# Kernel tuning notes

Measured on AMD Instinct MI355X. Metric: run time of the kernel, lower is better.

Reference implementation:

```python
import jax, jax.numpy as jnp
import numpy as np

S = 4        # support_num
NEI = 32     # neighbor_num for conv stages
POOL_NEI = 4 # neighbor_num inside Pool_layer
EPS = 1e-12


def sq_dist(a, b):
    # a: (b,m,3), b: (b,n,3) -> (b,m,n)
    return (jnp.sum(a * a, -1)[:, :, None] + jnp.sum(b * b, -1)[:, None, :]
            - 2.0 * jnp.einsum('bmd,bnd->bmn', a, b))


def query_ball(radius, k, points, queries):
    # PointNet++-style ball query: up to k indices within radius, padded with first hit.
    d = sq_dist(queries, points)                      # (b,m,n)
    n = points.shape[1]
    idx = jnp.broadcast_to(jnp.arange(n, dtype=jnp.int32), d.shape)
    idx = jnp.where(d > radius * radius, n, idx)
    idx = jnp.sort(idx, axis=-1)[..., :k]             # (b,m,k)
    first = idx[..., :1]
    return jnp.where(idx == n, first, idx)


def gather_nb(feat, idx):
    # feat: (b,v,c), idx: (b,v,k) -> (b,v,k,c)
    return jax.vmap(lambda f, i: f[i])(feat, idx)


def neighbor_dir_norm(verts, idx):
    nb = gather_nb(verts, idx)                        # (b,v,k,3)
    d = nb - verts[:, :, None, :]
    return d / (jnp.linalg.norm(d, axis=-1, keepdims=True) + EPS)


def conv_surface(idx, verts, dirs):
    # dirs: (3, S*out). Geometric-only first layer of 3DGCN.
    b, v, k = idx.shape
    o = dirs.shape[1] // S
    dn = neighbor_dir_norm(verts, idx)                # (b,v,k,3)
    sd = dirs / (jnp.linalg.norm(dirs, axis=0, keepdims=True) + EPS)
    theta = jnp.maximum(jnp.einsum('bvkd,dm->bvkm', dn, sd), 0.0)
    theta = theta.reshape(b, v, k, S, o)
    return theta.max(axis=2).sum(axis=2)              # (b,v,o)


def conv_layer(idx, verts, feat, w, bias, dirs):
    # w: (cin,(S+1)*o), bias: ((S+1)*o,), dirs: (3,S*o)
    b, v, k = idx.shape
    o = dirs.shape[1] // S
    dn = neighbor_dir_norm(verts, idx)
    sd = dirs / (jnp.linalg.norm(dirs, axis=0, keepdims=True) + EPS)
    theta = jnp.maximum(jnp.einsum('bvkd,dm->bvkm', dn, sd), 0.0)  # (b,v,k,S*o)
    fout = feat @ w + bias                            # (b,v,(S+1)*o)
    center, supp = fout[..., :o], fout[..., o:]
    supp_nb = gather_nb(supp, idx)                    # (b,v,k,S*o)
    act = (theta * supp_nb).reshape(b, v, k, S, o).max(axis=2).sum(axis=2)
    return center + act


def pool(verts, feat, radius):
    idx = query_ball(radius, POOL_NEI, verts, verts)
    pooled = gather_nb(feat, idx).max(axis=2)         # (b,v,c)
    m = verts.shape[1] // 2                           # pooling_rate = 2 (deterministic subsample)
    return verts[:, :m], pooled[:, :m]


def setup_inputs() -> dict:
    key = jax.random.key(0)
    ks = jax.random.split(key, 32)
    B, V = 4, 4096
    inp = {}
    inp['vertices'] = jax.random.uniform(ks[0], (B, V, 3), dtype=jnp.float32)
    inp['surf_dirs'] = jax.random.normal(ks[1], (3, S * 32), dtype=jnp.float32) * 0.1
    specs = [(1, 32, 32), (3, 64, 32), (4, 96, 32), (6, 128, 32), (7, 160, 32),
             (8, 192, 32), (9, 224, 32), (10, 256, 32), (11, 288, 1024)]
    i = 2
    for n, cin, cout in specs:
        inp[f'w{n}'] = jax.random.normal(ks[i], (cin, (S + 1) * cout), dtype=jnp.float32) / np.sqrt(cin); i += 1
        inp[f'b{n}'] = jnp.zeros(((S + 1) * cout,), jnp.float32)
        inp[f'd{n}'] = jax.random.normal(ks[i], (3, S * cout), dtype=jnp.float32) * 0.1; i += 1
    inp['fc1_w'] = jax.random.normal(ks[i], (1024, 256), dtype=jnp.float32) * 0.03; i += 1
    inp['fc1_b'] = jnp.zeros((256,), jnp.float32)
    inp['bn_g'] = jnp.ones((256,), jnp.float32)
    inp['bn_b'] = jnp.zeros((256,), jnp.float32)
    inp['bn_m'] = jnp.zeros((256,), jnp.float32)
    inp['bn_v'] = jnp.ones((256,), jnp.float32)
    inp['fc2_w'] = jax.random.normal(ks[i], (256, 40), dtype=jnp.float32) * 0.06
    inp['fc2_b'] = jnp.zeros((40,), jnp.float32)
    return inp


def reference(vertices, surf_dirs, w1, b1, d1, w3, b3, d3, w4, b4, d4, w6, b6, d6,
              w7, b7, d7, w8, b8, d8, w9, b9, d9, w10, b10, d10, w11, b11, d11,
              fc1_w, fc1_b, bn_g, bn_b, bn_m, bn_v, fc2_w, fc2_b):
    relu = lambda x: jnp.maximum(x, 0.0)
    verts = vertices
    idx = query_ball(0.2, NEI, verts, verts)
    fm0 = relu(conv_surface(idx, verts, surf_dirs))
    fm1 = relu(conv_layer(idx, verts, fm0, w1, b1, d1))
    fm1 = jnp.concatenate([fm0, fm1], -1)
    verts, fm1 = pool(verts, fm1, 0.2)
    idx = query_ball(0.4, NEI, verts, verts)
    fm3 = relu(conv_layer(idx, verts, fm1, w3, b3, d3)); fm3 = jnp.concatenate([fm1, fm3], -1)
    fm4 = relu(conv_layer(idx, verts, fm3, w4, b4, d4)); fm4 = jnp.concatenate([fm3, fm4], -1)
    verts, fm4 = pool(verts, fm4, 0.4)
    idx = query_ball(0.6, NEI, verts, verts)
    fm6 = relu(conv_layer(idx, verts, fm4, w6, b6, d6)); fm6 = jnp.concatenate([fm4, fm6], -1)
    fm7 = relu(conv_layer(idx, verts, fm6, w7, b7, d7)); fm7 = jnp.concatenate([fm6, fm7], -1)
    verts, fm7 = pool(verts, fm7, 0.6)
    idx = query_ball(0.8, NEI, verts, verts)
    fm8 = relu(conv_layer(idx, verts, fm7, w8, b8, d8)); fm8 = jnp.concatenate([fm7, fm8], -1)
    fm9 = relu(conv_layer(idx, verts, fm8, w9, b9, d9)); fm9 = jnp.concatenate([fm8, fm9], -1)
    verts, fm9 = pool(verts, fm9, 0.8)
    idx = query_ball(1.0, NEI, verts, verts)
    fm10 = relu(conv_layer(idx, verts, fm9, w10, b10, d10)); fm10 = jnp.concatenate([fm9, fm10], -1)
    fm11 = conv_layer(idx, verts, fm10, w11, b11, d11)
    g = fm11.max(axis=1)                              # (b,1024) global max pool
    h = g @ fc1_w + fc1_b                             # Dropout is identity at inference
    h = (h - bn_m) / jnp.sqrt(bn_v + 1e-5) * bn_g + bn_b
    h = relu(h)
    return h @ fc2_w + fc2_b                          # (b,40)
```

## Files before the change

### kernel.cpp

```cpp
#include <hip/hip_runtime.h>
#include <hip/hip_bf16.h>
#include <math.h>

#define DEV __device__ __forceinline__

DEV float frn_mul(float a, float b) { return __fmul_rn(a, b); }
DEV float frn_add(float a, float b) { return __fadd_rn(a, b); }

union BFU { __hip_bfloat16 h; unsigned short u; };

typedef __attribute__((ext_vector_type(8))) short short8v;
typedef __attribute__((ext_vector_type(4))) float f32x4;

__global__ void pack4_kernel(const float* __restrict__ v, float4* __restrict__ out,
                             int n)
{
    int t = blockIdx.x * blockDim.x + threadIdx.x;
    if (t >= n) return;
    float x = v[(size_t)t * 3 + 0], y = v[(size_t)t * 3 + 1], z = v[(size_t)t * 3 + 2];
    float pn = frn_add(frn_add(frn_mul(x, x), frn_mul(y, y)), frn_mul(z, z));
    out[t] = make_float4(x, y, z, pn);
}

__global__ void qb_kernel(const float4* __restrict__ pts4all, int Vp, int Vq, int B,
                          float r2, int K, int* __restrict__ idx_out)
{
    int wid = (blockIdx.x * blockDim.x + threadIdx.x) >> 6;
    int lane = threadIdx.x & 63;
    int nq = B * Vq;
    if (wid >= nq) return;
    int b = wid / Vq;
    int v = wid - b * Vq;

    float4 q4 = pts4all[(size_t)b * Vp + v];
    float qx = q4.x, qy = q4.y, qz = q4.z, qn = q4.w;
    const float4* pts = pts4all + (size_t)b * Vp;
    int* row = idx_out + (size_t)wid * K;

    int count = 0;
    int first = -1;
    float4 p = pts[lane];
    for (int base = 0; base < Vp && count < K; base += 64) {
        int jn = base + 64 + lane;
        float4 pnext = pts[jn < Vp ? jn : 0];
        float dt = frn_add(frn_add(frn_mul(qx, p.x), frn_mul(qy, p.y)), frn_mul(qz, p.z));
        float d = __fsub_rn(frn_add(qn, p.w), frn_mul(2.0f, dt));
        bool in = !(d > r2);
        unsigned long long mask = __ballot(in);
        if (first < 0 && mask != 0ull)
            first = base + (int)__ffsll((long long)mask) - 1;
        int pos = count + (int)__popcll(mask & ((1ull << lane) - 1ull));
        if (in && pos < K) row[pos] = base + lane;
        count += (int)__popcll(mask);
        p = pnext;
    }
    int cnt = count < K ? count : K;
    for (int t = cnt + lane; t < K; t += 64) row[t] = first;
}

__global__ void qb_surface_kernel(const float4* __restrict__ pts4all, int V, int B,
                                  float r2,
                                  const float* __restrict__ dirs,
                                  float* __restrict__ outF, int Cw,
                                  int* __restrict__ idx_out)
{
    __shared__ int rowS[4][32];
    int wid = (blockIdx.x * blockDim.x + threadIdx.x) >> 6;
    int lane = threadIdx.x & 63;
    int wql = threadIdx.x >> 6;
    int b = wid / V;

    float4 q4 = pts4all[(size_t)wid];
    float qx = q4.x, qy = q4.y, qz = q4.z, qn = q4.w;
    const float4* pts = pts4all + (size_t)b * V;
    int* row = idx_out + (size_t)wid * 32;

    int count = 0;
    int first = -1;
    float4 p = pts[lane];
    for (int base = 0; base < V && count < 32; base += 64) {
        int jn = base + 64 + lane;
        float4 pnext = pts[jn < V ? jn : 0];
        float dt = frn_add(frn_add(frn_mul(qx, p.x), frn_mul(qy, p.y)), frn_mul(qz, p.z));
        float d = __fsub_rn(frn_add(qn, p.w), frn_mul(2.0f, dt));
        bool in = !(d > r2);
        unsigned long long mask = __ballot(in);
        if (first < 0 && mask != 0ull)
            first = base + (int)__ffsll((long long)mask) - 1;
        int pos = count + (int)__popcll(mask & ((1ull << lane) - 1ull));
        if (in && pos < 32) { row[pos] = base + lane; rowS[wql][pos] = base + lane; }
        count += (int)__popcll(mask);
        p = pnext;
    }
    int cnt = count < 32 ? count : 32;
    for (int t = cnt + lane; t < 32; t += 64) { row[t] = first; rowS[wql][t] = first; }
    __syncthreads();

    float dnx, dny, dnz;
    {
        int k = lane & 31;
        float4 nb4 = pts[rowS[wql][k]];
        float dx = nb4.x - qx;
        float dy = nb4.y - qy;
        float dz = nb4.z - qz;
        float nrm = sqrtf(dx * dx + dy * dy + dz * dz) + 1e-12f;
        float inv = 1.0f / nrm;
        dnx = dx * inv; dny = dy * inv; dnz = dz * inv;
    }
    int m1 = lane, m2 = lane + 64;
    float ax = dirs[m1], ay = dirs[128 + m1], az = dirs[256 + m1];
    float i1 = 1.0f / (sqrtf(ax * ax + ay * ay + az * az) + 1e-12f);
    ax *= i1; ay *= i1; az *= i1;
    float bx = dirs[m2], by = dirs[128 + m2], bz = dirs[256 + m2];
    float i2 = 1.0f / (sqrtf(bx * bx + by * by + bz * bz) + 1e-12f);
    bx *= i2; by *= i2; bz *= i2;

    float mx1 = -INFINITY, mx2 = -INFINITY;
    for (int k = 0; k < 32; ++k) {
        float ex = __shfl(dnx, k, 64);
        float ey = __shfl(dny, k, 64);
        float ez = __shfl(dnz, k, 64);
        float t1 = fmaxf(ex * ax + ey * ay + ez * az, 0.0f);
        float t2 = fmaxf(ex * bx + ey * by + ez * bz, 0.0f);
        mx1 = fmaxf(mx1, t1);
        mx2 = fmaxf(mx2, t2);
    }
    float part = mx1 + mx2;
    float tot = part + __shfl_xor(part, 32, 64);
    if (lane < 32) {
        outF[(size_t)wid * Cw + lane] = fmaxf(tot, 0.0f);
    }
}

template <typename OT>
__global__ __launch_bounds__(256)
void gemm_tiled_kernel(const float* __restrict__ feat, int Cw, int cin,
                       const float* __restrict__ w, const float* __restrict__ bias,
                       int N, OT* __restrict__ fout)
{
    __shared__ float As[64][36];
    __shared__ float Bs[32][68];

    int m0 = blockIdx.x * 64;
    int n0 = blockIdx.y * 64;
    int tid = threadIdx.x;
    int tx = tid & 15, ty = tid >> 4;

    float acc[4][4];
#pragma unroll
    for (int i = 0; i < 4; ++i)
#pragma unroll
        for (int j = 0; j < 4; ++j) acc[i][j] = 0.0f;

    for (int k0 = 0; k0 < cin; k0 += 32) {
#pragma unroll
        for (int i = 0; i < 2; ++i) {
            int qq = tid + i * 256;
            int row = qq >> 3, c = qq & 7;
            float4 v = *(const float4*)&feat[(size_t)(m0 + row) * Cw + k0 + 4 * c];
            *(float4*)&As[row][4 * c] = v;
        }
#pragma unroll
        for (int i = 0; i < 2; ++i) {
            int qq = tid + i * 256;
            int kr = qq >> 4, c = qq & 15;
            int n = n0 + 4 * c;
            float4 v = make_float4(0.0f, 0.0f, 0.0f, 0.0f);
            if (n < N) v = *(const float4*)&w[(size_t)(k0 + kr) * N + n];
            *(float4*)&Bs[kr][4 * c] = v;
        }
        __syncthreads();

#pragma unroll
        for (int kt = 0; kt < 32; kt += 4) {
            float4 av4[4], bv4[4];
#pragma unroll
            for (int i = 0; i < 4; ++i) av4[i] = *(const float4*)&As[ty * 4 + i][kt];
#pragma unroll
            for (int r = 0; r < 4; ++r) bv4[r] = *(const float4*)&Bs[kt + r][tx * 4];
            const float* a = (const float*)av4;
            const float* bb = (const float*)bv4;
#pragma unroll
            for (int i = 0; i < 4; ++i)
#pragma unroll
                for (int r = 0; r < 4; ++r)
#pragma unroll
                    for (int j = 0; j < 4; ++j)
                        acc[i][j] = fmaf(a[i * 4 + r], bb[r * 4 + j], acc[i][j]);
        }
        __syncthreads();
    }

    int n = n0 + tx * 4;
    if (n < N) {
        float b0 = bias[n + 0], b1 = bias[n + 1], b2 = bias[n + 2], b3 = bias[n + 3];
#pragma unroll
        for (int i = 0; i < 4; ++i) {
            int m = m0 + ty * 4 + i;
            if constexpr (__is_same(OT, float)) {
                float4 o;
                o.x = acc[i][0] + b0;
                o.y = acc[i][1] + b1;
                o.z = acc[i][2] + b2;
                o.w = acc[i][3] + b3;
                *(float4*)&fout[(size_t)m * N + n] = o;
            } else {
                BFU t0, t1, t2, t3;
                t0.h = __float2bfloat16(acc[i][0] + b0);
                t1.h = __float2bfloat16(acc[i][1] + b1);
                t2.h = __float2bfloat16(acc[i][2] + b2);
                t3.h = __float2bfloat16(acc[i][3] + b3);
                ushort4 o;
                o.x = t0.u; o.y = t1.u; o.z = t2.u; o.w = t3.u;
                *(ushort4*)&fout[(size_t)m * N + n] = o;
            }
        }
    }
}

__global__ void cast_bf16_kernel(const float* __restrict__ src,
                                 unsigned short* __restrict__ dst, int n8)
{
    int t = blockIdx.x * blockDim.x + threadIdx.x;
    if (t >= n8) return;
    float4 v0 = *(const float4*)&src[(size_t)t * 8];
    float4 v1 = *(const float4*)&src[(size_t)t * 8 + 4];
    BFU a;
    ushort4 o0, o1;
    a.h = __float2bfloat16(v0.x); o0.x = a.u;
    a.h = __float2bfloat16(v0.y); o0.y = a.u;
    a.h = __float2bfloat16(v0.z); o0.z = a.u;
    a.h = __float2bfloat16(v0.w); o0.w = a.u;
    a.h = __float2bfloat16(v1.x); o1.x = a.u;
    a.h = __float2bfloat16(v1.y); o1.y = a.u;
    a.h = __float2bfloat16(v1.z); o1.z = a.u;
    a.h = __float2bfloat16(v1.w); o1.w = a.u;
    *(ushort4*)&dst[(size_t)t * 8] = o0;
    *(ushort4*)&dst[(size_t)t * 8 + 4] = o1;
}

__global__ void castT_bf16_kernel(const float* __restrict__ w,
                                  unsigned short* __restrict__ wt)
{
    int t = blockIdx.x * blockDim.x + threadIdx.x;
    if (t >= 5120 * 36) return;
    int kc = t / 5120;
    int n = t - kc * 5120;
    BFU a;
    ushort4 o0, o1;
    a.h = __float2bfloat16(w[(size_t)(kc * 8 + 0) * 5120 + n]); o0.x = a.u;
    a.h = __float2bfloat16(w[(size_t)(kc * 8 + 1) * 5120 + n]); o0.y = a.u;
    a.h = __float2bfloat16(w[(size_t)(kc * 8 + 2) * 5120 + n]); o0.z = a.u;
    a.h = __float2bfloat16(w[(size_t)(kc * 8 + 3) * 5120 + n]); o0.w = a.u;
    a.h = __float2bfloat16(w[(size_t)(kc * 8 + 4) * 5120 + n]); o1.x = a.u;
    a.h = __float2bfloat16(w[(size_t)(kc * 8 + 5) * 5120 + n]); o1.y = a.u;
    a.h = __float2bfloat16(w[(size_t)(kc * 8 + 6) * 5120 + n]); o1.z = a.u;
    a.h = __float2bfloat16(w[(size_t)(kc * 8 + 7) * 5120 + n]); o1.w = a.u;
    *(ushort4*)&wt[(size_t)n * 288 + kc * 8] = o0;
    *(ushort4*)&wt[(size_t)n * 288 + kc * 8 + 4] = o1;
}

__global__ __launch_bounds__(256)
void gemm_mfma_conv11(const unsigned short* __restrict__ Abf,
                      const unsigned short* __restrict__ WTbf,
                      const float* __restrict__ bias,
                      __hip_bfloat16* __restrict__ fout)
{
    __shared__ unsigned short As[128][40];
    __shared__ unsigned short Bs[128][40];
    const int K = 288, N = 5120;
    int m0 = blockIdx.x * 128;
    int n0 = blockIdx.y * 128;
    int tid = threadIdx.x;
    int lane = tid & 63;
    int wave = tid >> 6;
    int wm = wave & 1, wn = wave >> 1;
    int l15 = lane & 15, l4 = lane >> 4;

    f32x4 acc[4][4];
#pragma unroll
    for (int mi = 0; mi < 4; ++mi)
#pragma unroll
        for (int ni = 0; ni < 4; ++ni) acc[mi][ni] = (f32x4){0.f, 0.f, 0.f, 0.f};

    for (int k0 = 0; k0 < K; k0 += 32) {
#pragma unroll
        for (int i = 0; i < 2; ++i) {
            int c = tid + i * 256;
            int row = c >> 2, qq = c & 3;
            *(uint4*)&As[row][qq * 8] = *(const uint4*)&Abf[(size_t)(m0 + row) * K + k0 + qq * 8];
            *(uint4*)&Bs[row][qq * 8] = *(const uint4*)&WTbf[(size_t)(n0 + row) * K + k0 + qq * 8];
        }
        __syncthreads();

        short8v af[4], bfv[4];
#pragma unroll
        for (int mi = 0; mi < 4; ++mi)
            af[mi] = *(const short8v*)&As[wm * 64 + mi * 16 + l15][l4 * 8];
#pragma unroll
        for (int ni = 0; ni < 4; ++ni)
            bfv[ni] = *(const short8v*)&Bs[wn * 64 + ni * 16 + l15][l4 * 8];
#pragma unroll
        for (int mi = 0; mi < 4; ++mi)
#pragma unroll
            for (int ni = 0; ni < 4; ++ni)
                acc[mi][ni] = __builtin_amdgcn_mfma_f32_16x16x32_bf16(af[mi], bfv[ni], acc[mi][ni], 0, 0, 0);
        __syncthreads();
    }

#pragma unroll
    for (int ni = 0; ni < 4; ++ni) {
        int col = n0 + wn * 64 + ni * 16 + l15;
        float bv = bias[col];
#pragma unroll
        for (int mi = 0; mi < 4; ++mi) {
            int rbase = m0 + wm * 64 + mi * 16 + l4 * 4;
#pragma unroll
            for (int j = 0; j < 4; ++j) {
                BFU u;
                u.h = __float2bfloat16(acc[mi][ni][j] + bv);
                *(unsigned short*)&fout[(size_t)(rbase + j) * N + col] = u.u;
            }
        }
    }
}

__global__ void conv_agg32_kernel(const int* __restrict__ idx,
                                  const float4* __restrict__ verts4,
                                  const float* __restrict__ fout,
                                  const float* __restrict__ dirs,
                                  float* __restrict__ outF, int Cw, int coff,
                                  int V, int do_relu)
{
    int blk = blockIdx.x;
    int b = (blk & 7) >> 1;
    int j = ((blk >> 3) << 1) | (blk & 1);
    int wid = b * V + j * 4 + (int)(threadIdx.x >> 6);
    int lane = threadIdx.x & 63;

    float dnx, dny, dnz;
    int nbrow;
    {
        int k = lane & 31;
        int nb = idx[(size_t)wid * 32 + k];
        nbrow = b * V + nb;
        float4 c4 = verts4[(size_t)wid];
        float4 n4 = verts4[(size_t)nbrow];
        float dx = n4.x - c4.x;
        float dy = n4.y - c4.y;
        float dz = n4.z - c4.z;
        float nrm = sqrtf(dx * dx + dy * dy + dz * dz) + 1e-12f;
        float inv = 1.0f / nrm;
        dnx = dx * inv; dny = dy * inv; dnz = dz * inv;
    }
    int m1 = lane, m2 = lane + 64;
    float ax = dirs[m1], ay = dirs[128 + m1], az = dirs[256 + m1];
    float i1 = 1.0f / (sqrtf(ax * ax + ay * ay + az * az) + 1e-12f);
    ax *= i1; ay *= i1; az *= i1;
    float bx = dirs[m2], by = dirs[128 + m2], bz = dirs[256 + m2];
    float i2 = 1.0f / (sqrtf(bx * bx + by * by + bz * bz) + 1e-12f);
    bx *= i2; by *= i2; bz *= i2;

    float a1[4] = {-INFINITY, -INFINITY, -INFINITY, -INFINITY};
    float a2[4] = {-INFINITY, -INFINITY, -INFINITY, -INFINITY};
#pragma unroll
    for (int kk = 0; kk < 32; kk += 4) {
#pragma unroll
        for (int u = 0; u < 4; ++u) {
            int k = kk + u;
            float ex = __shfl(dnx, k, 64);
            float ey = __shfl(dny, k, 64);
            float ez = __shfl(dnz, k, 64);
            int nr = __shfl(nbrow, k, 64);
            const float* fr = fout + (size_t)nr * 160 + 32;
            float t1 = fmaxf(ex * ax + ey * ay + ez * az, 0.0f);
            float t2 = fmaxf(ex * bx + ey * by + ez * bz, 0.0f);
            a1[u] = fmaxf(a1[u], t1 * fr[m1]);
            a2[u] = fmaxf(a2[u], t2 * fr[m2]);
        }
    }
    float mx1 = fmaxf(fmaxf(a1[0], a1[1]), fmaxf(a1[2], a1[3]));
    float mx2 = fmaxf(fmaxf(a2[0], a2[1]), fmaxf(a2[2], a2[3]));
    float part = mx1 + mx2;
    float tot = part + __shfl_xor(part, 32, 64);
    if (lane < 32) {
        float c = fout[(size_t)wid * 160 + lane];
        float val = c + tot;
        if (do_relu) val = fmaxf(val, 0.0f);
        outF[(size_t)wid * Cw + coff + lane] = val;
    }
}

__global__ void conv_agg_big_kernel(const int* __restrict__ idx,
                                    const float4* __restrict__ verts4,
                                    const __hip_bfloat16* __restrict__ fout,
                                    const float* __restrict__ dirs,
                                    float* __restrict__ G,
                                    int V, int B)
{
    __shared__ float dnS[32][3];
    __shared__ int nbS[32];
    int blk = blockIdx.x;
    int b = (blk & 7) >> 1;
    int v = ((blk >> 3) << 1) | (blk & 1);
    int row = b * V + v;
    int tid = threadIdx.x;

    if (tid < 32) {
        int nb = idx[(size_t)row * 32 + tid];
        int nbrow = b * V + nb;
        float4 c4 = verts4[(size_t)row];
        float4 n4 = verts4[(size_t)nbrow];
        float dx = n4.x - c4.x;
        float dy = n4.y - c4.y;
        float dz = n4.z - c4.z;
        float nrm = sqrtf(dx * dx + dy * dy + dz * dz) + 1e-12f;
        float inv = 1.0f / nrm;
        dnS[tid][0] = dx * inv; dnS[tid][1] = dy * inv; dnS[tid][2] = dz * inv;
        nbS[tid] = nbrow;
    }
    __syncthreads();

    float sdx[16], sdy[16], sdz[16], mx[16];
    for (int p = 0; p < 16; ++p) {
        int pair = p * 256 + tid;
        float ax = dirs[pair], ay = dirs[4096 + pair], az = dirs[8192 + pair];
        float inv = 1.0f / (sqrtf(ax * ax + ay * ay + az * az) + 1e-12f);
        sdx[p] = ax * inv; sdy[p] = ay * inv; sdz[p] = az * inv;
        mx[p] = -INFINITY;
    }
    for (int k = 0; k < 32; ++k) {
        float ex = dnS[k][0], ey = dnS[k][1], ez = dnS[k][2];
        const __hip_bfloat16* fr = fout + (size_t)nbS[k] * 5120 + 1024;
        for (int p = 0; p < 16; ++p) {
            float th = fmaxf(ex * sdx[p] + ey * sdy[p] + ez * sdz[p], 0.0f);
            float s = __bfloat162float(fr[p * 256 + tid]);
            mx[p] = fmaxf(mx[p], th * s);
        }
    }
    for (int q = 0; q < 4; ++q) {
        float val = ((mx[q] + mx[4 + q]) + mx[8 + q]) + mx[12 + q];
        int oo = q * 256 + tid;
        float c = __bfloat162float(fout[(size_t)row * 5120 + oo]);
        G[(size_t)row * 1024 + oo] = c + val;
    }
}

__global__ void pool_fused_kernel(const int* __restrict__ idx_conv,
                                  const float4* __restrict__ verts4, int Vp, int Vh, int B,
                                  const float* __restrict__ Fin, int CwIn,
                                  float* __restrict__ Fout, int CwOut, int C,
                                  float4* __restrict__ vout4)
{
    int wid = (blockIdx.x * blockDim.x + threadIdx.x) >> 6;
    int lane = threadIdx.x & 63;
    int nq = B * Vh;
    if (wid >= nq) return;
    int b = wid / Vh;
    int v = wid - b * Vh;
    int rowc = b * Vp + v;

    int idv = 0;
    if (lane < 4) idv = idx_conv[(size_t)rowc * 32 + lane];
    int i0 = __shfl(idv, 0, 64);
    int i1 = __shfl(idv, 1, 64);
    int i2 = __shfl(idv, 2, 64);
    int i3 = __shfl(idv, 3, 64);

    const float* r0 = Fin + (size_t)(b * Vp + i0) * CwIn;
    const float* r1 = Fin + (size_t)(b * Vp + i1) * CwIn;
    const float* r2p = Fin + (size_t)(b * Vp + i2) * CwIn;
    const float* r3 = Fin + (size_t)(b * Vp + i3) * CwIn;
    for (int c = lane; c < C; c += 64) {
        float m = fmaxf(fmaxf(r0[c], r1[c]), fmaxf(r2p[c], r3[c]));
        Fout[(size_t)wid * CwOut + c] = m;
    }
    if (lane == 0) vout4[(size_t)wid] = verts4[(size_t)rowc];
}

__global__ void gmax_kernel(const float* __restrict__ G, float* __restrict__ gm,
                            int V)
{
    __shared__ float red[4][64];
    int b = blockIdx.x >> 4;
    int c0 = (blockIdx.x & 15) * 64;
    int t = threadIdx.x;
    int c = c0 + (t & 63);
    int vg = t >> 6;
    float m = -INFINITY;
    for (int v = vg * 64; v < (vg + 1) * 64; ++v)
        m = fmaxf(m, G[((size_t)b * V + v) * 1024 + c]);
    red[vg][t & 63] = m;
    __syncthreads();
    if (t < 64) {
        float r = fmaxf(fmaxf(red[0][t], red[1][t]), fmaxf(red[2][t], red[3][t]));
        gm[b * 1024 + c0 + t] = r;
    }
}

__global__ __launch_bounds__(256)
void fc1_kernel(const float* __restrict__ gm, const float* __restrict__ w1,
                const float* __restrict__ b1_,
                const float* __restrict__ bn_g, const float* __restrict__ bn_b,
                const float* __restrict__ bn_m, const float* __restrict__ bn_v,
                float* __restrict__ h)
{
    __shared__ float gs[1024];
    __shared__ float red[8][32];
    int b = blockIdx.y;
    int j0 = blockIdx.x * 32;
    int t = threadIdx.x;
    for (int i = t; i < 1024; i += 256) gs[i] = gm[b * 1024 + i];
    __syncthreads();
    int jj = t & 31, kk = t >> 5;
    int j = j0 + jj;
    const float* wp = w1 + (size_t)(kk * 128) * 256 + j;
    float acc = 0.0f;
#pragma unroll 8
    for (int k = 0; k < 128; ++k)
        acc = fmaf(gs[kk * 128 + k], wp[(size_t)k * 256], acc);
    red[kk][jj] = acc;
    __syncthreads();
    if (t < 32) {
        float s = 0.0f;
#pragma unroll
        for (int q = 0; q < 8; ++q) s += red[q][t];
        int jw = j0 + t;
        s += b1_[jw];
        s = (s - bn_m[jw]) / sqrtf(bn_v[jw] + 1e-5f) * bn_g[jw] + bn_b[jw];
        h[b * 256 + jw] = fmaxf(s, 0.0f);
    }
}

__global__ void fc2_kernel(const float* __restrict__ h, const float* __restrict__ w2,
                           const float* __restrict__ b2_, float* __restrict__ out)
{
    __shared__ float hs[256];
    int b = blockIdx.x;
    int t = threadIdx.x;
    hs[t] = h[b * 256 + t];
    __syncthreads();
    if (t < 40) {
        float acc = 0.0f;
#pragma unroll 8
        for (int k = 0; k < 256; ++k) acc = fmaf(hs[k], w2[(size_t)k * 40 + t], acc);
        out[b * 40 + t] = acc + b2_[t];
    }
}

static inline int wblocks(int waves) { return (waves + 3) / 4; }
static inline int tblocks(int threads) { return (threads + 255) / 256; }
static inline dim3 ggrid(int M, int N) { return dim3(M / 64, (N + 63) / 64); }

extern "C" void kernel_launch(void* const* d_in, const int* in_sizes, int n_in,
                              void* d_out, int out_size, void* d_ws, size_t ws_size,
                              hipStream_t stream)
{
    const int B = 4;
    const float* verts1 = (const float*)d_in[0];
    const float* surf_dirs = (const float*)d_in[1];
    const float* w1 = (const float*)d_in[2];
    const float* b1 = (const float*)d_in[3];
    const float* d1 = (const float*)d_in[4];
    const float* w3 = (const float*)d_in[5];
    const float* b3 = (const float*)d_in[6];
    const float* d3 = (const float*)d_in[7];
    const float* w4 = (const float*)d_in[8];
    const float* b4 = (const float*)d_in[9];
    const float* d4 = (const float*)d_in[10];
    const float* w6 = (const float*)d_in[11];
    const float* b6 = (const float*)d_in[12];
    const float* d6 = (const float*)d_in[13];
    const float* w7 = (const float*)d_in[14];
    const float* b7 = (const float*)d_in[15];
    const float* d7 = (const float*)d_in[16];
    const float* w8 = (const float*)d_in[17];
    const float* b8 = (const float*)d_in[18];
    const float* d8 = (const float*)d_in[19];
    const float* w9 = (const float*)d_in[20];
    const float* b9 = (const float*)d_in[21];
    const float* d9 = (const float*)d_in[22];
    const float* w10 = (const float*)d_in[23];
    const float* b10 = (const float*)d_in[24];
    const float* d10 = (const float*)d_in[25];
    const float* w11 = (const float*)d_in[26];
    const float* b11 = (const float*)d_in[27];
    const float* d11 = (const float*)d_in[28];
    const float* fc1_w = (const float*)d_in[29];
    const float* fc1_b = (const float*)d_in[30];
    const float* bn_g = (const float*)d_in[31];
    const float* bn_b = (const float*)d_in[32];
    const float* bn_m = (const float*)d_in[33];
    const float* bn_v = (const float*)d_in[34];
    const float* fc2_w = (const float*)d_in[35];
    const float* fc2_b = (const float*)d_in[36];
    (void)in_sizes; (void)n_in; (void)out_size; (void)ws_size;

    float* ws = (float*)d_ws;
    size_t off = 0;
    auto alloc = [&](size_t n) { float* p = ws + off; off += n; return p; };
    float* fout = alloc(4 * 256 * 5120);
    int* idx = (int*)alloc(4 * 4096 * 32);
    float* F1 = alloc(4 * 4096 * 64);
    float* L2 = alloc(4 * 2048 * 128);
    float* L3 = alloc(4 * 1024 * 192);
    float* L4 = alloc(4 * 512 * 256);
    float* L5 = alloc(4 * 256 * 288);
    float* G = alloc(4 * 256 * 1024);
    float4* vp1 = (float4*)alloc(4 * 4096 * 4);
    float4* v2 = (float4*)alloc(4 * 2048 * 4);
    float4* v3 = (float4*)alloc(4 * 1024 * 4);
    float4* v4 = (float4*)alloc(4 * 512 * 4);
    float4* v5 = (float4*)alloc(4 * 256 * 4);
    float* gm = alloc(4 * 1024);
    float* hh = alloc(4 * 256);

    unsigned short* Abf = (unsigned short*)G;
    unsigned short* WTbf = Abf + 1024 * 288;

    pack4_kernel<<<tblocks(B * 4096), 256, 0, stream>>>(verts1, vp1, B * 4096);
    qb_surface_kernel<<<wblocks(B * 4096), 256, 0, stream>>>(vp1, 4096, B, 0.04f, surf_dirs, F1, 64, idx);
    gemm_tiled_kernel<float><<<ggrid(B * 4096, 160), 256, 0, stream>>>(F1, 64, 32, w1, b1, 160, fout);
    conv_agg32_kernel<<<B * 4096 / 4, 256, 0, stream>>>(idx, vp1, fout, d1, F1, 64, 32, 4096, 1);
    pool_fused_kernel<<<wblocks(B * 2048), 256, 0, stream>>>(idx, vp1, 4096, 2048, B, F1, 64, L2, 128, 64, v2);

    qb_kernel<<<wblocks(B * 2048), 256, 0, stream>>>(v2, 2048, 2048, B, 0.16f, 32, idx);
    gemm_tiled_kernel<float><<<ggrid(B * 2048, 160), 256, 0, stream>>>(L2, 128, 64, w3, b3, 160, fout);
    conv_agg32_kernel<<<B * 2048 / 4, 256, 0, stream>>>(idx, v2, fout, d3, L2, 128, 64, 2048, 1);
    gemm_tiled_kernel<float><<<ggrid(B * 2048, 160), 256, 0, stream>>>(L2, 128, 96, w4, b4, 160, fout);
    conv_agg32_kernel<<<B * 2048 / 4, 256, 0, stream>>>(idx, v2, fout, d4, L2, 128, 96, 2048, 1);
    pool_fused_kernel<<<wblocks(B * 1024), 256, 0, stream>>>(idx, v2, 2048, 1024, B, L2, 128, L3, 192, 128, v3);

    qb_kernel<<<wblocks(B * 1024), 256, 0, stream>>>(v3, 1024, 1024, B, 0.36f, 32, idx);
    gemm_tiled_kernel<float><<<ggrid(B * 1024, 160), 256, 0, stream>>>(L3, 192, 128, w6, b6, 160, fout);
    conv_agg32_kernel<<<B * 1024 / 4, 256, 0, stream>>>(idx, v3, fout, d6, L3, 192, 128, 1024, 1);
    gemm_tiled_kernel<float><<<ggrid(B * 1024, 160), 256, 0, stream>>>(L3, 192, 160, w7, b7, 160, fout);
    conv_agg32_kernel<<<B * 1024 / 4, 256, 0, stream>>>(idx, v3, fout, d7, L3, 192, 160, 1024, 1);
    pool_fused_kernel<<<wblocks(B * 512), 256, 0, stream>>>(idx, v3, 1024, 512, B, L3, 192, L4, 256, 192, v4);

    qb_kernel<<<wblocks(B * 512), 256, 0, stream>>>(v4, 512, 512, B, 0.64f, 32, idx);
    gemm_tiled_kernel<float><<<ggrid(B * 512, 160), 256, 0, stream>>>(L4, 256, 192, w8, b8, 160, fout);
    conv_agg32_kernel<<<B * 512 / 4, 256, 0, stream>>>(idx, v4, fout, d8, L4, 256, 192, 512, 1);
    gemm_tiled_kernel<float><<<ggrid(B * 512, 160), 256, 0, stream>>>(L4, 256, 224, w9, b9, 160, fout);
    conv_agg32_kernel<<<B * 512 / 4, 256, 0, stream>>>(idx, v4, fout, d9, L4, 256, 224, 512, 1);
    pool_fused_kernel<<<wblocks(B * 256), 256, 0, stream>>>(idx, v4, 512, 256, B, L4, 256, L5, 288, 256, v5);

    qb_kernel<<<wblocks(B * 256), 256, 0, stream>>>(v5, 256, 256, B, 1.0f, 32, idx);
    castT_bf16_kernel<<<(5120 * 36 + 255) / 256, 256, 0, stream>>>(w11, WTbf);
    gemm_tiled_kernel<float><<<ggrid(B * 256, 160), 256, 0, stream>>>(L5, 288, 256, w10, b10, 160, fout);
    conv_agg32_kernel<<<B * 256 / 4, 256, 0, stream>>>(idx, v5, fout, d10, L5, 288, 256, 256, 1);
    cast_bf16_kernel<<<(36864 + 255) / 256, 256, 0, stream>>>(L5, Abf, 36864);
    __hip_bfloat16* fout_bf = (__hip_bfloat16*)fout;
    gemm_mfma_conv11<<<dim3(8, 40), 256, 0, stream>>>(Abf, WTbf, b11, fout_bf);
    conv_agg_big_kernel<<<B * 256, 256, 0, stream>>>(idx, v5, fout_bf, d11, G, 256, B);

    gmax_kernel<<<64, 256, 0, stream>>>(G, gm, 256);
    fc1_kernel<<<dim3(8, B), 256, 0, stream>>>(gm, fc1_w, fc1_b, bn_g, bn_b, bn_m, bn_v, hh);
    fc2_kernel<<<B, 256, 0, stream>>>(hh, fc2_w, fc2_b, (float*)d_out);
}
```

Measured before the change: 444.8 us.

## Vectorize conv_agg_big support loads and unroll ball-query scan loops

The big aggregation kernel now gives each thread 16 contiguous support channels instead of a stride-256 pattern. Each neighbor's support features are loaded as two 128-bit bf16 vectors and unpacked with bit shifts. Because the thread-to-channel mapping changed, the per-support maxima are staged through padded shared memory so the four supports can be summed per output channel. The ball-query kernels also unroll their scan by 2 or 4 chunks of 64 points with deeper prefetching. The cost is extra shared memory and a block barrier, and the loop may scan past the point where K hits are found.

```diff
diff --git a/kernel.cpp b/kernel.cpp
--- a/kernel.cpp
+++ b/kernel.cpp
@@ -39,20 +39,25 @@
 
     int count = 0;
     int first = -1;
-    float4 p = pts[lane];
-    for (int base = 0; base < Vp && count < K; base += 64) {
-        int jn = base + 64 + lane;
-        float4 pnext = pts[jn < Vp ? jn : 0];
-        float dt = frn_add(frn_add(frn_mul(qx, p.x), frn_mul(qy, p.y)), frn_mul(qz, p.z));
-        float d = __fsub_rn(frn_add(qn, p.w), frn_mul(2.0f, dt));
-        bool in = !(d > r2);
-        unsigned long long mask = __ballot(in);
-        if (first < 0 && mask != 0ull)
-            first = base + (int)__ffsll((long long)mask) - 1;
-        int pos = count + (int)__popcll(mask & ((1ull << lane) - 1ull));
-        if (in && pos < K) row[pos] = base + lane;
-        count += (int)__popcll(mask);
-        p = pnext;
+    float4 pbuf[2];
+#pragma unroll
+    for (int u = 0; u < 2; ++u) pbuf[u] = pts[u * 64 + lane];
+    for (int base = 0; base < Vp && count < K; base += 128) {
+#pragma unroll
+        for (int u = 0; u < 2; ++u) {
+            float4 p = pbuf[u];
+            int jn = base + 128 + u * 64 + lane;
+            pbuf[u] = pts[jn < Vp ? jn : 0];
+            float dt = frn_add(frn_add(frn_mul(qx, p.x), frn_mul(qy, p.y)), frn_mul(qz, p.z));
+            float d = __fsub_rn(frn_add(qn, p.w), frn_mul(2.0f, dt));
+            bool in = !(d > r2);
+            unsigned long long mask = __ballot(in);
+            if (first < 0 && mask != 0ull)
+                first = base + u * 64 + (int)__ffsll((long long)mask) - 1;
+            int pos = count + (int)__popcll(mask & ((1ull << lane) - 1ull));
+            if (in && pos < K) row[pos] = base + u * 64 + lane;
+            count += (int)__popcll(mask);
+        }
     }
     int cnt = count < K ? count : K;
     for (int t = cnt + lane; t < K; t += 64) row[t] = first;
@@ -77,20 +82,25 @@
 
     int count = 0;
     int first = -1;
-    float4 p = pts[lane];
-    for (int base = 0; base < V && count < 32; base += 64) {
-        int jn = base + 64 + lane;
-        float4 pnext = pts[jn < V ? jn : 0];
-        float dt = frn_add(frn_add(frn_mul(qx, p.x), frn_mul(qy, p.y)), frn_mul(qz, p.z));
-        float d = __fsub_rn(frn_add(qn, p.w), frn_mul(2.0f, dt));
-        bool in = !(d > r2);
-        unsigned long long mask = __ballot(in);
-        if (first < 0 && mask != 0ull)
-            first = base + (int)__ffsll((long long)mask) - 1;
-        int pos = count + (int)__popcll(mask & ((1ull << lane) - 1ull));
-        if (in && pos < 32) { row[pos] = base + lane; rowS[wql][pos] = base + lane; }
-        count += (int)__popcll(mask);
-        p = pnext;
+    float4 pbuf[4];
+#pragma unroll
+    for (int u = 0; u < 4; ++u) pbuf[u] = pts[u * 64 + lane];
+    for (int base = 0; base < V && count < 32; base += 256) {
+#pragma unroll
+        for (int u = 0; u < 4; ++u) {
+            float4 p = pbuf[u];
+            int jn = base + 256 + u * 64 + lane;
+            pbuf[u] = pts[jn < V ? jn : 0];
+            float dt = frn_add(frn_add(frn_mul(qx, p.x), frn_mul(qy, p.y)), frn_mul(qz, p.z));
+            float d = __fsub_rn(frn_add(qn, p.w), frn_mul(2.0f, dt));
+            bool in = !(d > r2);
+            unsigned long long mask = __ballot(in);
+            if (first < 0 && mask != 0ull)
+                first = base + u * 64 + (int)__ffsll((long long)mask) - 1;
+            int pos = count + (int)__popcll(mask & ((1ull << lane) - 1ull));
+            if (in && pos < 32) { row[pos] = base + u * 64 + lane; rowS[wql][pos] = base + u * 64 + lane; }
+            count += (int)__popcll(mask);
+        }
     }
     int cnt = count < 32 ? count : 32;
     for (int t = cnt + lane; t < 32; t += 64) { row[t] = first; rowS[wql][t] = first; }
@@ -391,15 +401,17 @@
     }
 }
 
-__global__ void conv_agg_big_kernel(const int* __restrict__ idx,
-                                    const float4* __restrict__ verts4,
-                                    const __hip_bfloat16* __restrict__ fout,
-                                    const float* __restrict__ dirs,
-                                    float* __restrict__ G,
-                                    int V, int B)
+__global__ __launch_bounds__(256)
+void conv_agg_big_kernel(const int* __restrict__ idx,
+                         const float4* __restrict__ verts4,
+                         const __hip_bfloat16* __restrict__ fout,
+                         const float* __restrict__ dirs,
+                         float* __restrict__ G,
+                         int V, int B)
 {
     __shared__ float dnS[32][3];
     __shared__ int nbS[32];
+    __shared__ float sm[256 * 17];
     int blk = blockIdx.x;
     int b = (blk & 7) >> 1;
     int v = ((blk >> 3) << 1) | (blk & 1);
@@ -421,26 +433,57 @@
     }
     __syncthreads();
 
+    int p0 = tid * 16;
+    float4 X[4], Y[4], Z[4];
+#pragma unroll
+    for (int c = 0; c < 4; ++c) {
+        X[c] = *(const float4*)&dirs[p0 + 4 * c];
+        Y[c] = *(const float4*)&dirs[4096 + p0 + 4 * c];
+        Z[c] = *(const float4*)&dirs[8192 + p0 + 4 * c];
+    }
+    const float* xf = (const float*)X;
+    const float* yf = (const float*)Y;
+    const float* zf = (const float*)Z;
     float sdx[16], sdy[16], sdz[16], mx[16];
+#pragma unroll
     for (int p = 0; p < 16; ++p) {
-        int pair = p * 256 + tid;
-        float ax = dirs[pair], ay = dirs[4096 + pair], az = dirs[8192 + pair];
+        float ax = xf[p], ay = yf[p], az = zf[p];
         float inv = 1.0f / (sqrtf(ax * ax + ay * ay + az * az) + 1e-12f);
         sdx[p] = ax * inv; sdy[p] = ay * inv; sdz[p] = az * inv;
         mx[p] = -INFINITY;
     }
+
     for (int k = 0; k < 32; ++k) {
         float ex = dnS[k][0], ey = dnS[k][1], ez = dnS[k][2];
         const __hip_bfloat16* fr = fout + (size_t)nbS[k] * 5120 + 1024;
-        for (int p = 0; p < 16; ++p) {
-            float th = fmaxf(ex * sdx[p] + ey * sdy[p] + ez * sdz[p], 0.0f);
-            float s = __bfloat162float(fr[p * 256 + tid]);
-            mx[p] = fmaxf(mx[p], th * s);
-        }
-    }
+        uint4 u0 = *(const uint4*)&fr[p0];
+        uint4 u1 = *(const uint4*)&fr[p0 + 8];
+        unsigned int uu[8] = {u0.x, u0.y, u0.z, u0.w, u1.x, u1.y, u1.z, u1.w};
+#pragma unroll
+        for (int h = 0; h < 8; ++h) {
+            float slo = __uint_as_float(uu[h] << 16);
+            float shi = __uint_as_float(uu[h] & 0xFFFF0000u);
+            int p = 2 * h;
+            float th0 = fmaxf(ex * sdx[p] + ey * sdy[p] + ez * sdz[p], 0.0f);
+            float th1 = fmaxf(ex * sdx[p + 1] + ey * sdy[p + 1] + ez * sdz[p + 1], 0.0f);
+            mx[p] = fmaxf(mx[p], th0 * slo);
+            mx[p + 1] = fmaxf(mx[p + 1], th1 * shi);
+        }
+    }
+
+#pragma unroll
+    for (int p = 0; p < 16; ++p) sm[tid * 17 + p] = mx[p];
+    __syncthreads();
+
+#pragma unroll
     for (int q = 0; q < 4; ++q) {
-        float val = ((mx[q] + mx[4 + q]) + mx[8 + q]) + mx[12 + q];
         int oo = q * 256 + tid;
+        int t0 = oo >> 4, pp = oo & 15;
+        float s0 = sm[t0 * 17 + pp];
+        float s1 = sm[(64 + t0) * 17 + pp];
+        float s2 = sm[(128 + t0) * 17 + pp];
+        float s3 = sm[(192 + t0) * 17 + pp];
+        float val = ((s0 + s1) + s2) + s3;
         float c = __bfloat162float(fout[(size_t)row * 5120 + oo]);
         G[(size_t)row * 1024 + oo] = c + val;
     }
```

Measured after the change: 440.4 us. Within noise of the previous version (-1.0%).
